# Kernel tuning notes

Hardware: AMD Instinct MI355X
Metric: run time of the kernel (lower is better)

## Reference

```python
import jax, jax.numpy as jnp
import numpy as np

EMB = 1024
HEADS = 16
HEAD_DIM = EMB // HEADS
D_FF = 4 * EMB
EPS = 1e-5


def setup_inputs() -> dict:
    key = jax.random.key(0)
    ks = jax.random.split(key, 12)
    b, t = 4, 2048
    sc = 0.02
    return {
        "x": jax.random.normal(ks[0], (b, t, EMB), dtype=jnp.float32),
        # weights stored [in, out] (transpose of torch Linear.weight)
        "w_attn": jax.random.normal(ks[1], (EMB, 3 * EMB), dtype=jnp.float32) * sc,
        "b_attn": jnp.zeros((3 * EMB,), dtype=jnp.float32),
        "w_proj": jax.random.normal(ks[2], (EMB, EMB), dtype=jnp.float32) * sc,
        "b_proj": jnp.zeros((EMB,), dtype=jnp.float32),
        "ln1_g": jnp.ones((EMB,), dtype=jnp.float32),
        "ln1_b": jnp.zeros((EMB,), dtype=jnp.float32),
        "w_ff1": jax.random.normal(ks[3], (EMB, D_FF), dtype=jnp.float32) * sc,
        "b_ff1": jnp.zeros((D_FF,), dtype=jnp.float32),
        "w_ff2": jax.random.normal(ks[4], (D_FF, EMB), dtype=jnp.float32) * sc,
        "b_ff2": jnp.zeros((EMB,), dtype=jnp.float32),
        "ln2_g": jnp.ones((EMB,), dtype=jnp.float32),
        "ln2_b": jnp.zeros((EMB,), dtype=jnp.float32),
    }


def _layernorm(x, g, b):
    mu = jnp.mean(x, axis=-1, keepdims=True)
    var = jnp.var(x, axis=-1, keepdims=True)
    return (x - mu) * jax.lax.rsqrt(var + EPS) * g + b


def reference(x, w_attn, b_attn, w_proj, b_proj, ln1_g, ln1_b,
              w_ff1, b_ff1, w_ff2, b_ff2, ln2_g, ln2_b):
    b, t, e = x.shape
    h, s = HEADS, HEAD_DIM
    # fused qkv projection (GPT2-style c_attn)
    qkv = x @ w_attn + b_attn                      # [b, t, 3e]
    q, k, v = jnp.split(qkv, 3, axis=-1)
    q = q.reshape(b, t, h, s).transpose(0, 2, 1, 3)  # [b, h, t, s]
    k = k.reshape(b, t, h, s).transpose(0, 2, 1, 3)
    v = v.reshape(b, t, h, s).transpose(0, 2, 1, 3)
    dot = jnp.einsum('bhqs,bhks->bhqk', q, k) / jnp.sqrt(jnp.float32(s))
    # causal mask: mask_(..., mask_diagonal=False) zeroes i < j (strict upper)
    causal = jnp.tril(jnp.ones((t, t), dtype=bool))
    dot = jnp.where(causal, dot, jnp.float32(-jnp.inf))
    att = jax.nn.softmax(dot, axis=-1)
    out = jnp.einsum('bhqk,bhks->bhqs', att, v)    # [b, h, t, s]
    out = out.transpose(0, 2, 1, 3).reshape(b, t, e)
    attended = out @ w_proj + b_proj
    # residual + LayerNorm (dropout is identity in eval mode)
    x1 = _layernorm(attended + x, ln1_g, ln1_b)
    ff = jax.nn.relu(x1 @ w_ff1 + b_ff1) @ w_ff2 + b_ff2
    return _layernorm(ff + x1, ln2_g, ln2_b)
```

## Files before the change

### kernel.cpp

```cpp
#include <hip/hip_runtime.h>
#include <hip/hip_bf16.h>


typedef __attribute__((ext_vector_type(8))) short bf16x8;
typedef __attribute__((ext_vector_type(4))) float f32x4;

__device__ __forceinline__ unsigned short f2b(float f) {
  unsigned int u = __float_as_uint(f);
  u += 0x7fffu + ((u >> 16) & 1u);
  return (unsigned short)(u >> 16);
}
__device__ __forceinline__ unsigned int pk2b(float a, float b) {
  __hip_bfloat162 h = __float22bfloat162_rn(make_float2(a, b));
  return *(unsigned int*)&h;
}
__device__ __forceinline__ void gload_lds16(const unsigned short* g, unsigned short* l) {
  __builtin_amdgcn_global_load_lds((const __attribute__((address_space(1))) void*)g,
                                   (__attribute__((address_space(3))) void*)l, 16, 0, 0);
}

__global__ __launch_bounds__(256) void cvt_bf16(const float* __restrict__ in,
                                                unsigned short* __restrict__ out, long n) {
  long i = ((long)blockIdx.x * 256 + threadIdx.x) * 4;
  if (i >= n) return;
  float4 v = *(const float4*)(in + i);
  *(ushort4*)(out + i) = make_ushort4(f2b(v.x), f2b(v.y), f2b(v.z), f2b(v.w));
}

__global__ __launch_bounds__(256) void transpose_bf16(const float* __restrict__ in,
                                                      unsigned short* __restrict__ out,
                                                      int R, int C) {
  __shared__ float tile[32][33];
  int c0 = blockIdx.x * 32, r0 = blockIdx.y * 32;
  for (int i = threadIdx.y; i < 32; i += 8)
    tile[i][threadIdx.x] = in[(long)(r0 + i) * C + c0 + threadIdx.x];
  __syncthreads();
  for (int i = threadIdx.y; i < 32; i += 8)
    out[(long)(c0 + i) * R + r0 + threadIdx.x] = f2b(tile[threadIdx.x][i]);
}

template <int EPI>
__global__ __launch_bounds__(512, 2) void gemm256(const unsigned short* __restrict__ A,
                                                  const unsigned short* __restrict__ Bt,
                                                  const float* __restrict__ bias,
                                                  void* __restrict__ Cout,
                                                  void* __restrict__ Cout2,
                                                  int N, int K, int Kstride) {
  __shared__ __align__(16) unsigned short As[4][256 * 32];
  __shared__ __align__(16) unsigned short Bs[4][256 * 32];

  int tid = threadIdx.x;
  int wv = tid >> 6, lane = tid & 63, quad = lane >> 4, l16 = lane & 15;
  int wm = wv >> 2, wn = wv & 3;

  int nwg = gridDim.x, id = blockIdx.x;
  int sid = (id & 7) * (nwg >> 3) + (id >> 3);
  int bm256 = (sid & 31) * 256, bn256 = (sid >> 5) * 256;
  int chunk = blockIdx.y;
  long kbase = (long)chunk * K;

  int row1 = tid >> 2, row2 = row1 + 128;
  long dsl = ((tid & 3) ^ ((tid >> 3) & 3)) * 8;
  const unsigned short* Ap1 = A + (long)(bm256 + row1) * Kstride + kbase + dsl;
  const unsigned short* Ap2 = A + (long)(bm256 + row2) * Kstride + kbase + dsl;
  const unsigned short* Bp1 = Bt + (long)(bn256 + row1) * Kstride + kbase + dsl;
  const unsigned short* Bp2 = Bt + (long)(bn256 + row2) * Kstride + kbase + dsl;
  int lo1 = wv * 512, lo2 = wv * 512 + 4096;

  f32x4 acc[8][4] = {};
  int sl8 = (quad ^ ((l16 >> 1) & 3)) * 8;
  int arow = wm * 128 + l16;
  int brow = wn * 64 + l16;

  int NT = K >> 5;
  gload_lds16(Ap1, &As[0][lo1]); gload_lds16(Ap2, &As[0][lo2]);
  gload_lds16(Bp1, &Bs[0][lo1]); gload_lds16(Bp2, &Bs[0][lo2]);
  gload_lds16(Ap1 + 32, &As[1][lo1]); gload_lds16(Ap2 + 32, &As[1][lo2]);
  gload_lds16(Bp1 + 32, &Bs[1][lo1]); gload_lds16(Bp2 + 32, &Bs[1][lo2]);
  gload_lds16(Ap1 + 64, &As[2][lo1]); gload_lds16(Ap2 + 64, &As[2][lo2]);
  asm volatile("s_waitcnt vmcnt(6)\n\ts_barrier" ::: "memory");
  __builtin_amdgcn_sched_barrier(0);

  for (int tau = 0; tau < NT; ++tau) {
    const unsigned short* Ab = &As[tau & 3][0];
    const unsigned short* Bb = &Bs[tau & 3][0];
    bf16x8 af[4], bfr[4];
#pragma unroll
    for (int i = 0; i < 4; ++i)
      af[i] = *(const bf16x8*)(Ab + (arow + i * 16) * 32 + sl8);
#pragma unroll
    for (int j = 0; j < 4; ++j)
      bfr[j] = *(const bf16x8*)(Bb + (brow + j * 16) * 32 + sl8);
    if (tau + 2 < NT) {
      long ko = (long)(tau + 2) * 32;
      int s = (tau + 2) & 3;
      gload_lds16(Bp1 + ko, &Bs[s][lo1]);
      gload_lds16(Bp2 + ko, &Bs[s][lo2]);
    }
    asm volatile("s_barrier\n\ts_waitcnt lgkmcnt(0)" ::: "memory");
    __builtin_amdgcn_sched_barrier(0);
    __builtin_amdgcn_s_setprio(1);
#pragma unroll
    for (int i = 0; i < 4; ++i)
#pragma unroll
      for (int j = 0; j < 4; ++j)
        acc[i][j] = __builtin_amdgcn_mfma_f32_16x16x32_bf16(af[i], bfr[j], acc[i][j], 0, 0, 0);
    __builtin_amdgcn_s_setprio(0);
    __builtin_amdgcn_s_barrier();
    __builtin_amdgcn_sched_barrier(0);
    bf16x8 ag[4];
#pragma unroll
    for (int i = 0; i < 4; ++i)
      ag[i] = *(const bf16x8*)(Ab + (arow + (i + 4) * 16) * 32 + sl8);
    if (tau + 3 < NT) {
      long ko = (long)(tau + 3) * 32;
      int s = (tau + 3) & 3;
      gload_lds16(Ap1 + ko, &As[s][lo1]);
      gload_lds16(Ap2 + ko, &As[s][lo2]);
    }
    asm volatile("s_barrier\n\ts_waitcnt lgkmcnt(0)" ::: "memory");
    __builtin_amdgcn_sched_barrier(0);
    __builtin_amdgcn_s_setprio(1);
#pragma unroll
    for (int i = 0; i < 4; ++i)
#pragma unroll
      for (int j = 0; j < 4; ++j)
        acc[i + 4][j] = __builtin_amdgcn_mfma_f32_16x16x32_bf16(ag[i], bfr[j], acc[i + 4][j], 0, 0, 0);
    __builtin_amdgcn_s_setprio(0);
    if (tau + 3 < NT) {
      asm volatile("s_waitcnt vmcnt(6)\n\ts_barrier" ::: "memory");
    } else if (tau + 2 < NT) {
      asm volatile("s_waitcnt vmcnt(4)\n\ts_barrier" ::: "memory");
    } else if (tau + 1 < NT) {
      asm volatile("s_waitcnt vmcnt(0)\n\ts_barrier" ::: "memory");
    }
    __builtin_amdgcn_sched_barrier(0);
  }

  void* Cbase = chunk ? Cout2 : Cout;
#pragma unroll
  for (int i = 0; i < 8; ++i) {
#pragma unroll
    for (int j = 0; j < 4; ++j) {
      int gn = bn256 + wn * 64 + j * 16 + l16;
      float bv = chunk ? 0.f : bias[gn];
      if (EPI == 3 && gn >= 2048) {
        int h = (gn >> 6) & 15, s = gn & 63;
        int gm0 = bm256 + wm * 128 + i * 16 + quad * 4;
        int b = gm0 >> 11, tt0 = gm0 & 2047;
        unsigned short* vt = (unsigned short*)Cout + 16777216L;
        ushort4 us;
        us.x = f2b(acc[i][j][0] + bv);
        us.y = f2b(acc[i][j][1] + bv);
        us.z = f2b(acc[i][j][2] + bv);
        us.w = f2b(acc[i][j][3] + bv);
        *(ushort4*)(vt + (((long)(b * 16 + h)) * 64 + s) * 2048 + tt0) = us;
      } else {
#pragma unroll
        for (int r = 0; r < 4; ++r) {
          int gm = bm256 + wm * 128 + i * 16 + quad * 4 + r;
          float v = acc[i][j][r] + bv;
          if (EPI == 2) v = fmaxf(v, 0.f);
          if (EPI == 0) {
            ((float*)Cbase)[(long)gm * N + gn] = v;
          } else if (EPI == 2) {
            ((unsigned short*)Cbase)[(long)gm * N + gn] = f2b(v);
          } else {
            float sc = (gn < 1024) ? 0.18033688011112042f : 1.0f;
            ((unsigned short*)Cbase)[(long)gm * 2048 + gn] = f2b(v * sc);
          }
        }
      }
    }
  }
}

__global__ __launch_bounds__(256) void attn_mfma(const unsigned short* __restrict__ qkv,
                                                 unsigned short* __restrict__ outp) {
  __shared__ __align__(16) unsigned short Ks[2][64 * 64];
  __shared__ __align__(16) unsigned short Vts[2][64 * 64];
  int id = blockIdx.x;
  int qa = (id >> 3) & 15, qb = 31 - qa;
  int g = (id & 7) | ((id >> 7) << 3);
  int h = g & 15, b = g >> 4;
  int t = threadIdx.x;
  int w = t >> 6, lane = t & 63, quad = lane >> 4, l16 = lane & 15;
  const unsigned short* qg = qkv + (long)(b * 2048) * 2048 + h * 64;
  const unsigned short* kg = qg + 1024;
  const unsigned short* vg = qkv + 16777216L + (((long)(b * 16 + h)) * 64) * 2048;

  bf16x8 qfa[2], qfb[2];
#pragma unroll
  for (int ks = 0; ks < 2; ++ks) {
    qfa[ks] = *(const bf16x8*)(qg + (long)(qa * 64 + w * 16 + l16) * 2048 + ks * 32 + quad * 8);
    qfb[ks] = *(const bf16x8*)(qg + (long)(qb * 64 + w * 16 + l16) * 2048 + ks * 32 + quad * 8);
  }

  int sr = t >> 2, c4 = t & 3;
  int fsr = (sr & 3) | (((sr >> 3) & 1) << 2);
  int ws0 = sr * 64 + (((2 * c4) ^ fsr) * 8);
  int ws1 = sr * 64 + (((2 * c4 + 1) ^ fsr) * 8);
  const unsigned short* kp = kg + (long)sr * 2048 + c4 * 16;
  const unsigned short* vp = vg + (long)sr * 2048 + c4 * 16;
  int4 kv0 = *(const int4*)kp, kv1 = *(const int4*)(kp + 8);
  int4 vv0 = *(const int4*)vp, vv1 = *(const int4*)(vp + 8);
  kp += (long)64 * 2048;
  vp += 64;

  f32x4 oa[4] = {}, ob[4] = {};
  f32x4 la = {}, lb = {};
  const short ONE = 0x3F80;
  bf16x8 ones = {ONE, ONE, ONE, ONE, ONE, ONE, ONE, ONE};

  int fs = l16 & 7;
  int fv = (l16 & 3) | (((l16 >> 3) & 1) << 2);
  int qrow = w * 16 + l16;

  auto process = [&](const bf16x8 (&qf)[2], bool diag,
                     f32x4 (&oacc)[4], f32x4& lacc,
                     const unsigned short* Kb, const unsigned short* Vb) {
#pragma unroll
    for (int kc = 0; kc < 2; ++kc) {
      unsigned int apw[4];
#pragma unroll
      for (int aa = 0; aa < 2; ++aa) {
        int row = 8 * (l16 >> 2) + (l16 & 3) + 4 * aa + 32 * kc;
        const unsigned short* kr = Kb + row * 64;
        bf16x8 kf0 = *(const bf16x8*)(kr + (quad ^ fs) * 8);
        bf16x8 kf1 = *(const bf16x8*)(kr + ((quad ^ 4 ^ fs)) * 8);
        f32x4 st = {};
        st = __builtin_amdgcn_mfma_f32_16x16x32_bf16(kf0, qf[0], st, 0, 0, 0);
        st = __builtin_amdgcn_mfma_f32_16x16x32_bf16(kf1, qf[1], st, 0, 0, 0);
        if (diag) {
          int kq = 8 * quad + 4 * aa + 32 * kc;
#pragma unroll
          for (int r = 0; r < 4; ++r)
            if (kq + r > qrow) st[r] = -1e30f;
        }
        apw[aa * 2]     = pk2b(exp2f(st[0]), exp2f(st[1]));
        apw[aa * 2 + 1] = pk2b(exp2f(st[2]), exp2f(st[3]));
      }
      union { unsigned int u[4]; bf16x8 v; } ap;
#pragma unroll
      for (int u = 0; u < 4; ++u) ap.u[u] = apw[u];
      lacc = __builtin_amdgcn_mfma_f32_16x16x32_bf16(ap.v, ones, lacc, 0, 0, 0);
#pragma unroll
      for (int sg = 0; sg < 4; ++sg) {
        int vrow = sg * 16 + l16;
        bf16x8 vf = *(const bf16x8*)(Vb + vrow * 64 + (((4 * kc + quad) ^ fv) * 8));
        oacc[sg] = __builtin_amdgcn_mfma_f32_16x16x32_bf16(ap.v, vf, oacc[sg], 0, 0, 0);
      }
    }
  };

  int nkt = qb + 1;
  for (int kt = 0; kt < nkt; ++kt) {
    unsigned short* Kb = &Ks[kt & 1][0];
    unsigned short* Vb = &Vts[kt & 1][0];
    *(int4*)(Kb + ws0) = kv0;
    *(int4*)(Kb + ws1) = kv1;
    *(int4*)(Vb + ws0) = vv0;
    *(int4*)(Vb + ws1) = vv1;
    __syncthreads();
    if (kt + 1 < nkt) {
      kv0 = *(const int4*)kp; kv1 = *(const int4*)(kp + 8);
      vv0 = *(const int4*)vp; vv1 = *(const int4*)(vp + 8);
      kp += (long)64 * 2048;
      vp += 64;
    }
    process(qfb, kt == qb, ob, lb, Kb, Vb);
    if (kt <= qa) process(qfa, kt == qa, oa, la, Kb, Vb);
  }

  auto epi = [&](int qt, f32x4 (&oacc)[4], f32x4& lacc) {
#pragma unroll
    for (int r = 0; r < 4; ++r) {
      float invl = 1.f / lacc[r];
      int row = qt * 64 + w * 16 + quad * 4 + r;
      unsigned short* op = outp + ((long)(b * 2048 + row)) * 1024 + h * 64;
#pragma unroll
      for (int sg = 0; sg < 4; ++sg) op[sg * 16 + l16] = f2b(oacc[sg][r] * invl);
    }
  };
  epi(qa, oa, la);
  epi(qb, ob, lb);
}

__global__ __launch_bounds__(256) void ln_kernel(const float* __restrict__ a,
                                                 const float* __restrict__ a2,
                                                 const float* __restrict__ res,
                                                 const float* __restrict__ gam,
                                                 const float* __restrict__ bet,
                                                 float* __restrict__ outf,
                                                 unsigned short* __restrict__ outb) {
  int row = blockIdx.x, t = threadIdx.x;
  float4 av = *(const float4*)(a + (long)row * 1024 + t * 4);
  float4 rv = *(const float4*)(res + (long)row * 1024 + t * 4);
  float v0 = av.x + rv.x, v1 = av.y + rv.y, v2 = av.z + rv.z, v3 = av.w + rv.w;
  if (a2) {
    float4 a2v = *(const float4*)(a2 + (long)row * 1024 + t * 4);
    v0 += a2v.x; v1 += a2v.y; v2 += a2v.z; v3 += a2v.w;
  }
  float s = v0 + v1 + v2 + v3;
  float ss = v0 * v0 + v1 * v1 + v2 * v2 + v3 * v3;
#pragma unroll
  for (int off = 32; off >= 1; off >>= 1) {
    s += __shfl_down(s, off);
    ss += __shfl_down(ss, off);
  }
  __shared__ float sb[4], ssb[4];
  __shared__ float mean_s, inv_s;
  int w = t >> 6, lane = t & 63;
  if (lane == 0) { sb[w] = s; ssb[w] = ss; }
  __syncthreads();
  if (t == 0) {
    float S = sb[0] + sb[1] + sb[2] + sb[3];
    float SS = ssb[0] + ssb[1] + ssb[2] + ssb[3];
    float mean = S * (1.f / 1024.f);
    float var = SS * (1.f / 1024.f) - mean * mean;
    mean_s = mean;
    inv_s = rsqrtf(var + 1e-5f);
  }
  __syncthreads();
  float mean = mean_s, inv = inv_s;
  int c = t * 4;
  float4 gv = *(const float4*)(gam + c);
  float4 bv = *(const float4*)(bet + c);
  float y0 = (v0 - mean) * inv * gv.x + bv.x;
  float y1 = (v1 - mean) * inv * gv.y + bv.y;
  float y2 = (v2 - mean) * inv * gv.z + bv.z;
  float y3 = (v3 - mean) * inv * gv.w + bv.w;
  *(float4*)(outf + (long)row * 1024 + c) = make_float4(y0, y1, y2, y3);
  if (outb) {
    *(ushort4*)(outb + (long)row * 1024 + c) = make_ushort4(f2b(y0), f2b(y1), f2b(y2), f2b(y3));
  }
}

extern "C" void kernel_launch(void* const* d_in, const int* in_sizes, int n_in,
                              void* d_out, int out_size, void* d_ws, size_t ws_size,
                              hipStream_t stream) {
  const float* x      = (const float*)d_in[0];
  const float* w_attn = (const float*)d_in[1];
  const float* b_attn = (const float*)d_in[2];
  const float* w_proj = (const float*)d_in[3];
  const float* b_proj = (const float*)d_in[4];
  const float* ln1_g  = (const float*)d_in[5];
  const float* ln1_b  = (const float*)d_in[6];
  const float* w_ff1  = (const float*)d_in[7];
  const float* b_ff1  = (const float*)d_in[8];
  const float* w_ff2  = (const float*)d_in[9];
  const float* b_ff2  = (const float*)d_in[10];
  const float* ln2_g  = (const float*)d_in[11];
  const float* ln2_b  = (const float*)d_in[12];

  const long M = 8192, E = 1024;
  char* ws = (char*)d_ws;
  unsigned short* xb   = (unsigned short*)ws; ws += M * E * 2;
  unsigned short* wTa  = (unsigned short*)ws; ws += 3072L * 1024 * 2;
  unsigned short* wTp  = (unsigned short*)ws; ws += 1024L * 1024 * 2;
  unsigned short* wTf1 = (unsigned short*)ws; ws += 4096L * 1024 * 2;
  unsigned short* wTf2 = (unsigned short*)ws; ws += 4096L * 1024 * 2;
  unsigned short* qkvb = (unsigned short*)ws; ws += M * 3072 * 2;
  unsigned short* attb = (unsigned short*)ws; ws += M * E * 2;
  float* a1f = (float*)ws; ws += M * E * 4;
  float* x1f = (float*)ws; ws += M * E * 4;
  unsigned short* x1b = (unsigned short*)ws; ws += M * E * 2;
  unsigned short* hb = qkvb;
  float* f2 = a1f;
  float* prj1 = (float*)qkvb;
  float* ff21 = (float*)d_ws;

  cvt_bf16<<<dim3((M * E) / 4 / 256), dim3(256), 0, stream>>>(x, xb, M * E);
  transpose_bf16<<<dim3(3072 / 32, 1024 / 32), dim3(32, 8), 0, stream>>>(w_attn, wTa, 1024, 3072);
  transpose_bf16<<<dim3(1024 / 32, 1024 / 32), dim3(32, 8), 0, stream>>>(w_proj, wTp, 1024, 1024);
  transpose_bf16<<<dim3(4096 / 32, 1024 / 32), dim3(32, 8), 0, stream>>>(w_ff1, wTf1, 1024, 4096);
  transpose_bf16<<<dim3(1024 / 32, 4096 / 32), dim3(32, 8), 0, stream>>>(w_ff2, wTf2, 4096, 1024);
  gemm256<3><<<dim3(384, 1), dim3(512), 0, stream>>>(xb, wTa, b_attn, qkvb, nullptr, 3072, 1024, 1024);
  attn_mfma<<<dim3(1024), dim3(256), 0, stream>>>(qkvb, attb);
  gemm256<0><<<dim3(128, 2), dim3(512), 0, stream>>>(attb, wTp, b_proj, a1f, prj1, 1024, 512, 1024);
  ln_kernel<<<dim3(8192), dim3(256), 0, stream>>>(a1f, prj1, x, ln1_g, ln1_b, x1f, x1b);
  gemm256<2><<<dim3(512, 1), dim3(512), 0, stream>>>(x1b, wTf1, b_ff1, hb, nullptr, 4096, 1024, 1024);
  gemm256<0><<<dim3(128, 2), dim3(512), 0, stream>>>(hb, wTf2, b_ff2, f2, ff21, 1024, 2048, 4096);
  ln_kernel<<<dim3(8192), dim3(256), 0, stream>>>(f2, ff21, x1f, ln2_g, ln2_b, (float*)d_out, nullptr);
}
```

Baseline: 542.1 us.

## Split attention blocks to one query tile each, heaviest tiles first

The attention kernel previously paired a short and a long causal query tile per block so both reused the same K/V tiles and work was balanced. It now launches twice as many blocks, each handling one query tile, ordered from the longest causal range down. This halves the per-block accumulator state and may improve occupancy and tail scheduling. The cost is that K/V tiles are loaded and staged in LDS separately for each query tile, roughly doubling that traffic.

```diff
diff --git a/kernel.cpp b/kernel.cpp
--- a/kernel.cpp
+++ b/kernel.cpp
@@ -180,8 +180,8 @@
   __shared__ __align__(16) unsigned short Ks[2][64 * 64];
   __shared__ __align__(16) unsigned short Vts[2][64 * 64];
   int id = blockIdx.x;
-  int qa = (id >> 3) & 15, qb = 31 - qa;
-  int g = (id & 7) | ((id >> 7) << 3);
+  int g = (id & 7) | ((id >> 8) << 3);
+  int qi = 31 - ((id >> 3) & 31);
   int h = g & 15, b = g >> 4;
   int t = threadIdx.x;
   int w = t >> 6, lane = t & 63, quad = lane >> 4, l16 = lane & 15;
@@ -189,12 +189,10 @@
   const unsigned short* kg = qg + 1024;
   const unsigned short* vg = qkv + 16777216L + (((long)(b * 16 + h)) * 64) * 2048;
 
-  bf16x8 qfa[2], qfb[2];
-#pragma unroll
-  for (int ks = 0; ks < 2; ++ks) {
-    qfa[ks] = *(const bf16x8*)(qg + (long)(qa * 64 + w * 16 + l16) * 2048 + ks * 32 + quad * 8);
-    qfb[ks] = *(const bf16x8*)(qg + (long)(qb * 64 + w * 16 + l16) * 2048 + ks * 32 + quad * 8);
-  }
+  bf16x8 qf[2];
+#pragma unroll
+  for (int ks = 0; ks < 2; ++ks)
+    qf[ks] = *(const bf16x8*)(qg + (long)(qi * 64 + w * 16 + l16) * 2048 + ks * 32 + quad * 8);
 
   int sr = t >> 2, c4 = t & 3;
   int fsr = (sr & 3) | (((sr >> 3) & 1) << 2);
@@ -207,8 +205,8 @@
   kp += (long)64 * 2048;
   vp += 64;
 
-  f32x4 oa[4] = {}, ob[4] = {};
-  f32x4 la = {}, lb = {};
+  f32x4 oa[4] = {};
+  f32x4 la = {};
   const short ONE = 0x3F80;
   bf16x8 ones = {ONE, ONE, ONE, ONE, ONE, ONE, ONE, ONE};
 
@@ -216,44 +214,7 @@
   int fv = (l16 & 3) | (((l16 >> 3) & 1) << 2);
   int qrow = w * 16 + l16;
 
-  auto process = [&](const bf16x8 (&qf)[2], bool diag,
-                     f32x4 (&oacc)[4], f32x4& lacc,
-                     const unsigned short* Kb, const unsigned short* Vb) {
-#pragma unroll
-    for (int kc = 0; kc < 2; ++kc) {
-      unsigned int apw[4];
-#pragma unroll
-      for (int aa = 0; aa < 2; ++aa) {
-        int row = 8 * (l16 >> 2) + (l16 & 3) + 4 * aa + 32 * kc;
-        const unsigned short* kr = Kb + row * 64;
-        bf16x8 kf0 = *(const bf16x8*)(kr + (quad ^ fs) * 8);
-        bf16x8 kf1 = *(const bf16x8*)(kr + ((quad ^ 4 ^ fs)) * 8);
-        f32x4 st = {};
-        st = __builtin_amdgcn_mfma_f32_16x16x32_bf16(kf0, qf[0], st, 0, 0, 0);
-        st = __builtin_amdgcn_mfma_f32_16x16x32_bf16(kf1, qf[1], st, 0, 0, 0);
-        if (diag) {
-          int kq = 8 * quad + 4 * aa + 32 * kc;
-#pragma unroll
-          for (int r = 0; r < 4; ++r)
-            if (kq + r > qrow) st[r] = -1e30f;
-        }
-        apw[aa * 2]     = pk2b(exp2f(st[0]), exp2f(st[1]));
-        apw[aa * 2 + 1] = pk2b(exp2f(st[2]), exp2f(st[3]));
-      }
-      union { unsigned int u[4]; bf16x8 v; } ap;
-#pragma unroll
-      for (int u = 0; u < 4; ++u) ap.u[u] = apw[u];
-      lacc = __builtin_amdgcn_mfma_f32_16x16x32_bf16(ap.v, ones, lacc, 0, 0, 0);
-#pragma unroll
-      for (int sg = 0; sg < 4; ++sg) {
-        int vrow = sg * 16 + l16;
-        bf16x8 vf = *(const bf16x8*)(Vb + vrow * 64 + (((4 * kc + quad) ^ fv) * 8));
-        oacc[sg] = __builtin_amdgcn_mfma_f32_16x16x32_bf16(ap.v, vf, oacc[sg], 0, 0, 0);
-      }
-    }
-  };
-
-  int nkt = qb + 1;
+  int nkt = qi + 1;
   for (int kt = 0; kt < nkt; ++kt) {
     unsigned short* Kb = &Ks[kt & 1][0];
     unsigned short* Vb = &Vts[kt & 1][0];
@@ -268,22 +229,49 @@
       kp += (long)64 * 2048;
       vp += 64;
     }
-    process(qfb, kt == qb, ob, lb, Kb, Vb);
-    if (kt <= qa) process(qfa, kt == qa, oa, la, Kb, Vb);
-  }
-
-  auto epi = [&](int qt, f32x4 (&oacc)[4], f32x4& lacc) {
-#pragma unroll
-    for (int r = 0; r < 4; ++r) {
-      float invl = 1.f / lacc[r];
-      int row = qt * 64 + w * 16 + quad * 4 + r;
-      unsigned short* op = outp + ((long)(b * 2048 + row)) * 1024 + h * 64;
-#pragma unroll
-      for (int sg = 0; sg < 4; ++sg) op[sg * 16 + l16] = f2b(oacc[sg][r] * invl);
-    }
-  };
-  epi(qa, oa, la);
-  epi(qb, ob, lb);
+    bool diag = (kt == qi);
+#pragma unroll
+    for (int kc = 0; kc < 2; ++kc) {
+      unsigned int apw[4];
+#pragma unroll
+      for (int aa = 0; aa < 2; ++aa) {
+        int row = 8 * (l16 >> 2) + (l16 & 3) + 4 * aa + 32 * kc;
+        const unsigned short* kr = Kb + row * 64;
+        bf16x8 kf0 = *(const bf16x8*)(kr + (quad ^ fs) * 8);
+        bf16x8 kf1 = *(const bf16x8*)(kr + ((quad ^ 4 ^ fs)) * 8);
+        f32x4 st = {};
+        st = __builtin_amdgcn_mfma_f32_16x16x32_bf16(kf0, qf[0], st, 0, 0, 0);
+        st = __builtin_amdgcn_mfma_f32_16x16x32_bf16(kf1, qf[1], st, 0, 0, 0);
+        if (diag) {
+          int kq = 8 * quad + 4 * aa + 32 * kc;
+#pragma unroll
+          for (int r = 0; r < 4; ++r)
+            if (kq + r > qrow) st[r] = -1e30f;
+        }
+        apw[aa * 2]     = pk2b(exp2f(st[0]), exp2f(st[1]));
+        apw[aa * 2 + 1] = pk2b(exp2f(st[2]), exp2f(st[3]));
+      }
+      union { unsigned int u[4]; bf16x8 v; } ap;
+#pragma unroll
+      for (int u = 0; u < 4; ++u) ap.u[u] = apw[u];
+      la = __builtin_amdgcn_mfma_f32_16x16x32_bf16(ap.v, ones, la, 0, 0, 0);
+#pragma unroll
+      for (int sg = 0; sg < 4; ++sg) {
+        int vrow = sg * 16 + l16;
+        bf16x8 vf = *(const bf16x8*)(Vb + vrow * 64 + (((4 * kc + quad) ^ fv) * 8));
+        oa[sg] = __builtin_amdgcn_mfma_f32_16x16x32_bf16(ap.v, vf, oa[sg], 0, 0, 0);
+      }
+    }
+  }
+
+#pragma unroll
+  for (int r = 0; r < 4; ++r) {
+    float invl = 1.f / la[r];
+    int row = qi * 64 + w * 16 + quad * 4 + r;
+    unsigned short* op = outp + ((long)(b * 2048 + row)) * 1024 + h * 64;
+#pragma unroll
+    for (int sg = 0; sg < 4; ++sg) op[sg * 16 + l16] = f2b(oa[sg][r] * invl);
+  }
 }
 
 __global__ __launch_bounds__(256) void ln_kernel(const float* __restrict__ a,
@@ -376,7 +364,7 @@
   transpose_bf16<<<dim3(4096 / 32, 1024 / 32), dim3(32, 8), 0, stream>>>(w_ff1, wTf1, 1024, 4096);
   transpose_bf16<<<dim3(1024 / 32, 4096 / 32), dim3(32, 8), 0, stream>>>(w_ff2, wTf2, 4096, 1024);
   gemm256<3><<<dim3(384, 1), dim3(512), 0, stream>>>(xb, wTa, b_attn, qkvb, nullptr, 3072, 1024, 1024);
-  attn_mfma<<<dim3(1024), dim3(256), 0, stream>>>(qkvb, attb);
+  attn_mfma<<<dim3(2048), dim3(256), 0, stream>>>(qkvb, attb);
   gemm256<0><<<dim3(128, 2), dim3(512), 0, stream>>>(attb, wTp, b_proj, a1f, prj1, 1024, 512, 1024);
   ln_kernel<<<dim3(8192), dim3(256), 0, stream>>>(a1f, prj1, x, ln1_g, ln1_b, x1f, x1b);
   gemm256<2><<<dim3(512, 1), dim3(512), 0, stream>>>(x1b, wTf1, b_ff1, hb, nullptr, 4096, 1024, 1024);
```

New measurement: 561.4 us. 3.6% more time.
